# Performance work log

Measured on AMD Instinct MI355X. Metric: run time of the kernel, lower is better.

## Reference

```python
import jax, jax.numpy as jnp
import numpy as np

B, S, H = 8, 2048, 1024

def setup_inputs() -> dict:
    key = jax.random.key(0)
    k1, k2, k3, k4, k5, k6 = jax.random.split(key, 6)
    scale = 1.0 / np.sqrt(H)
    return {
        "hidden_states": jax.random.normal(k1, (B, S, H), dtype=jnp.float32),
        "key_padding_mask": jax.random.bernoulli(k2, 0.1, (B, S)),  # True = padded key
        "Wq_w": jax.random.normal(k3, (H, H), dtype=jnp.float32) * scale,
        "Wq_b": jax.random.normal(k4, (H,), dtype=jnp.float32) * 0.01,
        "Wk_w": jax.random.normal(k5, (H, H), dtype=jnp.float32) * scale,
        "Wk_b": jax.random.normal(k6, (H,), dtype=jnp.float32) * 0.01,
    }

def reference(hidden_states, key_padding_mask, Wq_w, Wq_b, Wk_w, Wk_b):
    # torch nn.Linear: y = x @ W.T + b
    q = jnp.einsum("bsh,oh->bso", hidden_states, Wq_w) + Wq_b
    k = jnp.einsum("bsh,oh->bso", hidden_states, Wk_w) + Wk_b
    d = q.shape[-1]
    scores = jnp.einsum("bqd,bkd->bqk", q, k) / jnp.sqrt(jnp.asarray(d, q.dtype))
    # scores[mask] -= inf  -> masked key columns become -inf
    scores = jnp.where(key_padding_mask[:, None, :], -jnp.inf, scores)
    attn = jax.nn.softmax(scores, axis=2)  # [B, S, S]
    out = jnp.einsum("bqk,bkd->bqd", attn, hidden_states)  # values = hidden_states (no proj)
    return out
```

## Files before the change

kernel.cpp:

```cpp
#include <hip/hip_runtime.h>
#include <hip/hip_bf16.h>

using bf16 = __hip_bfloat16;

using frag_ab = __attribute__((ext_vector_type(8))) short;
using frag_cd = __attribute__((ext_vector_type(4))) float;

#define TM 128
#define TN 128
#define TK 32

__device__ __forceinline__ unsigned short f2bu(float f) {
    bf16 h = __float2bfloat16(f);
    return *(unsigned short*)&h;
}

__device__ __forceinline__ void st_c(float* p, float v) { *p = v; }
__device__ __forceinline__ void st_c(bf16* p, float v)  { *p = __float2bfloat16(v); }

__device__ __forceinline__ void load16(const bf16* g, bf16* l) {
    __builtin_amdgcn_global_load_lds(
        (const __attribute__((address_space(1))) unsigned int*)g,
        (__attribute__((address_space(3))) unsigned int*)l,
        16, 0, 0);
}

template <typename TC, bool HAS_BIAS, bool MASK>
__global__ __launch_bounds__(256)
void mfma_gemm_nt(const bf16* __restrict__ A, const bf16* __restrict__ B,
                  const float* __restrict__ bias, const int* __restrict__ mask,
                  TC* __restrict__ C, int N, int K, int lda, int ldb, int ldc,
                  long sA, long sB, long sC, long sM, float scale)
{
    __shared__ bf16 As[2][TM][TK];
    __shared__ bf16 Bs[2][TN][TK];

    const int bz = blockIdx.z;
    const bf16* Ab = A + (long)bz * sA;
    const bf16* Bb = B + (long)bz * sB;
    TC* Cb = C + (long)bz * sC;
    const int* maskb = MASK ? (mask + (long)bz * sM) : nullptr;

    const int t  = threadIdx.x;
    const int m0 = blockIdx.x * TM;
    const int n0 = blockIdx.y * TN;

    const int srow  = t >> 2;
    const int skoff = (t & 3) << 3;
    const bf16* ga0 = Ab + (long)(m0 + srow) * lda + skoff;
    const bf16* ga1 = ga0 + (long)64 * lda;
    const bf16* gb0 = Bb + (long)(n0 + srow) * ldb + skoff;
    const bf16* gb1 = gb0 + (long)64 * ldb;

    const int wave = t >> 6;
    const int lane = t & 63;
    const int wm   = (wave & 1) * 64;
    const int wn   = (wave >> 1) * 64;
    const int lrow = lane & 15;
    const int quad = lane >> 4;

    frag_cd acc[4][4] = {};

#define STAGE(buf)                                         \
    do {                                                   \
        load16(ga0, &As[buf][srow][skoff]);                \
        load16(ga1, &As[buf][srow + 64][skoff]);           \
        load16(gb0, &Bs[buf][srow][skoff]);                \
        load16(gb1, &Bs[buf][srow + 64][skoff]);           \
        ga0 += TK; ga1 += TK; gb0 += TK; gb1 += TK;        \
    } while (0)

    STAGE(0);
    __syncthreads();

    int cur = 0;
    for (int k0 = 0; k0 < K; k0 += TK) {
        if (k0 + TK < K) STAGE(cur ^ 1);

        frag_ab af[4], bfv[4];
#pragma unroll
        for (int i = 0; i < 4; ++i)
            af[i] = *(const frag_ab*)&As[cur][wm + i * 16 + lrow][quad * 8];
#pragma unroll
        for (int j = 0; j < 4; ++j)
            bfv[j] = *(const frag_ab*)&Bs[cur][wn + j * 16 + lrow][quad * 8];
#pragma unroll
        for (int i = 0; i < 4; ++i)
#pragma unroll
            for (int j = 0; j < 4; ++j)
                acc[i][j] = __builtin_amdgcn_mfma_f32_16x16x32_bf16(
                    af[i], bfv[j], acc[i][j], 0, 0, 0);

        __syncthreads();
        cur ^= 1;
    }
#undef STAGE

#pragma unroll
    for (int j = 0; j < 4; ++j) {
        const int col = n0 + wn + j * 16 + lrow;
        const float bv = HAS_BIAS ? bias[col] : 0.0f;
        const bool msk = MASK ? (maskb[col] != 0) : false;
#pragma unroll
        for (int i = 0; i < 4; ++i) {
            const int rbase = m0 + wm + i * 16 + quad * 4;
#pragma unroll
            for (int r = 0; r < 4; ++r) {
                float v = acc[i][j][r] * scale + bv;
                if (MASK && msk) v = -INFINITY;
                st_c(&Cb[(long)(rbase + r) * ldc + col], v);
            }
        }
    }
}

__global__ __launch_bounds__(256)
void convert_transpose(const float* __restrict__ X, bf16* __restrict__ Xb,
                       bf16* __restrict__ XT, int S, int H)
{
    __shared__ unsigned short tile[64][72];
    const int b = blockIdx.z;
    const float* Xp = X + (long)b * S * H;
    bf16* Xbp = Xb + (long)b * S * H;
    bf16* XTp = XT + (long)b * H * S;
    const int h0 = blockIdx.x * 64, s0 = blockIdx.y * 64;
    const int t = threadIdx.x;
    const int r  = t >> 4;
    const int c4 = (t & 15) * 4;

#pragma unroll
    for (int p = 0; p < 4; ++p) {
        const int row = r + p * 16;
        const float4 v = *(const float4*)&Xp[(long)(s0 + row) * H + h0 + c4];
        ushort4 u;
        u.x = f2bu(v.x); u.y = f2bu(v.y); u.z = f2bu(v.z); u.w = f2bu(v.w);
        *(ushort4*)&tile[row][c4] = u;
        *(ushort4*)&Xbp[(long)(s0 + row) * H + h0 + c4] = u;
    }
    __syncthreads();
#pragma unroll
    for (int p = 0; p < 4; ++p) {
        const int hrow = r + p * 16;
        ushort4 u;
        u.x = tile[c4 + 0][hrow];
        u.y = tile[c4 + 1][hrow];
        u.z = tile[c4 + 2][hrow];
        u.w = tile[c4 + 3][hrow];
        *(ushort4*)&XTp[(long)(h0 + hrow) * S + s0 + c4] = u;
    }
}

__global__ __launch_bounds__(256)
void convert_bf16(const float* __restrict__ in, bf16* __restrict__ out, int n4)
{
    const int i = blockIdx.x * 256 + threadIdx.x;
    if (i < n4) {
        const float4 v = ((const float4*)in)[i];
        ushort4 u;
        u.x = f2bu(v.x); u.y = f2bu(v.y); u.z = f2bu(v.z); u.w = f2bu(v.w);
        ((ushort4*)out)[i] = u;
    }
}

__global__ __launch_bounds__(256)
void pack_bias(const float* __restrict__ qb, const float* __restrict__ kb,
               float* __restrict__ out, int H)
{
    const int i = blockIdx.x * 256 + threadIdx.x;
    out[i] = (i < H) ? qb[i] : kb[i - H];
}

__global__ __launch_bounds__(256)
void softmax_kernel(bf16* __restrict__ Smat, int Slen)
{
    const int row = blockIdx.x;
    bf16* srow = Smat + (long)row * Slen;

    const int t    = threadIdx.x;
    const int lane = t & 63;
    const int wid  = t >> 6;

    ushort4 u0 = ((const ushort4*)srow)[t * 2];
    ushort4 u1 = ((const ushort4*)srow)[t * 2 + 1];

    float vals[8];
    {
        const unsigned short us[8] = {u0.x, u0.y, u0.z, u0.w, u1.x, u1.y, u1.z, u1.w};
#pragma unroll
        for (int i = 0; i < 8; ++i) {
            unsigned int w = (unsigned int)us[i] << 16;
            vals[i] = *(float*)&w;
        }
    }

    float mx = vals[0];
#pragma unroll
    for (int i = 1; i < 8; ++i) mx = fmaxf(mx, vals[i]);

    __shared__ float red[4];
#pragma unroll
    for (int o = 32; o > 0; o >>= 1) mx = fmaxf(mx, __shfl_xor(mx, o, 64));
    if (lane == 0) red[wid] = mx;
    __syncthreads();
    mx = fmaxf(fmaxf(red[0], red[1]), fmaxf(red[2], red[3]));
    __syncthreads();

    float sum = 0.0f;
#pragma unroll
    for (int i = 0; i < 8; ++i) {
        const float e = __expf(vals[i] - mx);
        vals[i] = e;
        sum += e;
    }
#pragma unroll
    for (int o = 32; o > 0; o >>= 1) sum += __shfl_xor(sum, o, 64);
    if (lane == 0) red[wid] = sum;
    __syncthreads();
    sum = red[0] + red[1] + red[2] + red[3];

    const float inv = 1.0f / sum;
    ushort4 o0, o1;
    o0.x = f2bu(vals[0] * inv); o0.y = f2bu(vals[1] * inv);
    o0.z = f2bu(vals[2] * inv); o0.w = f2bu(vals[3] * inv);
    o1.x = f2bu(vals[4] * inv); o1.y = f2bu(vals[5] * inv);
    o1.z = f2bu(vals[6] * inv); o1.w = f2bu(vals[7] * inv);
    ((ushort4*)srow)[t * 2]     = o0;
    ((ushort4*)srow)[t * 2 + 1] = o1;
}

extern "C" void kernel_launch(void* const* d_in, const int* in_sizes, int n_in,
                              void* d_out, int out_size, void* d_ws, size_t ws_size,
                              hipStream_t stream)
{
    const float* hidden = (const float*)d_in[0];
    const int*   mask   = (const int*)d_in[1];
    const float* Wq_w   = (const float*)d_in[2];
    const float* Wq_b   = (const float*)d_in[3];
    const float* Wk_w   = (const float*)d_in[4];
    const float* Wk_b   = (const float*)d_in[5];
    float* out = (float*)d_out;

    const int B = 8, S = 2048, H = 1024;
    const int M = B * S;
    const long MH = (long)M * H;

    bf16* QK  = (bf16*)d_ws;
    bf16* XbT = QK + MH * 2;
    bf16* Sb  = XbT + MH;
    bf16* Xb  = Sb;
    bf16* Wb  = Xb + MH;
    float* biasP = (float*)(Wb + 2L * H * H);

    const dim3 blk(256);

    convert_transpose<<<dim3(H / 64, S / 64, B), blk, 0, stream>>>(hidden, Xb, XbT, S, H);
    convert_bf16<<<dim3(H * H / 1024), blk, 0, stream>>>(Wq_w, Wb, H * H / 4);
    convert_bf16<<<dim3(H * H / 1024), blk, 0, stream>>>(Wk_w, Wb + (long)H * H, H * H / 4);
    pack_bias<<<dim3(2 * H / 256), blk, 0, stream>>>(Wq_b, Wk_b, biasP, H);

    mfma_gemm_nt<bf16, true, false><<<dim3(M / TM, 2 * H / TN, 1), blk, 0, stream>>>(
        Xb, Wb, biasP, nullptr, QK, 2 * H, H, H, H, 2 * H, 0, 0, 0, 0, 1.0f);

    mfma_gemm_nt<bf16, false, true><<<dim3(S / TM, S / TN, B), blk, 0, stream>>>(
        QK, QK + H, nullptr, mask, Sb, S, H, 2 * H, 2 * H, S,
        (long)S * 2 * H, (long)S * 2 * H, (long)S * S, S, 1.0f / 32.0f);

    softmax_kernel<<<dim3(B * S), blk, 0, stream>>>(Sb, S);

    mfma_gemm_nt<float, false, false><<<dim3(S / TM, H / TN, B), blk, 0, stream>>>(
        Sb, XbT, nullptr, nullptr, out, H, S, S, S, H,
        (long)S * S, (long)H * S, (long)S * H, 0, 1.0f);
}
```

Baseline: 455.7 us.

## Swizzle GEMM shared-memory tiles, raise occupancy hint, merge weight conversions

Applies an XOR-like rotation to the 16-byte chunk index when staging A/B tiles into LDS via global_load_lds, and reads fragments with the matching rotated offset, to reduce LDS bank conflicts on the MFMA fragment loads. Adds a min-blocks-per-CU hint of 4 to the GEMM launch bounds, which may force register limits. Merges the two weight conversion kernels into one launch to save launch overhead. The swizzle must stay consistent between writer and reader or results break.

After: 415.9 us. -8.7%, faster.

```diff
diff --git a/kernel.cpp b/kernel.cpp
--- a/kernel.cpp
+++ b/kernel.cpp
@@ -26,7 +26,7 @@
 }
 
 template <typename TC, bool HAS_BIAS, bool MASK>
-__global__ __launch_bounds__(256)
+__global__ __launch_bounds__(256, 4)
 void mfma_gemm_nt(const bf16* __restrict__ A, const bf16* __restrict__ B,
                   const float* __restrict__ bias, const int* __restrict__ mask,
                   TC* __restrict__ C, int N, int K, int lda, int ldb, int ldc,
@@ -45,11 +45,13 @@
     const int m0 = blockIdx.x * TM;
     const int n0 = blockIdx.y * TN;
 
-    const int srow  = t >> 2;
-    const int skoff = (t & 3) << 3;
-    const bf16* ga0 = Ab + (long)(m0 + srow) * lda + skoff;
+    const int srow = t >> 2;
+    const int c    = t & 3;
+    const int gco  = (((c - (srow >> 1)) & 3) << 3);
+    const int lco  = c << 3;
+    const bf16* ga0 = Ab + (long)(m0 + srow) * lda + gco;
     const bf16* ga1 = ga0 + (long)64 * lda;
-    const bf16* gb0 = Bb + (long)(n0 + srow) * ldb + skoff;
+    const bf16* gb0 = Bb + (long)(n0 + srow) * ldb + gco;
     const bf16* gb1 = gb0 + (long)64 * ldb;
 
     const int wave = t >> 6;
@@ -58,15 +60,16 @@
     const int wn   = (wave >> 1) * 64;
     const int lrow = lane & 15;
     const int quad = lane >> 4;
+    const int rco  = (((quad + (lrow >> 1)) & 3) << 3);
 
     frag_cd acc[4][4] = {};
 
 #define STAGE(buf)                                         \
     do {                                                   \
-        load16(ga0, &As[buf][srow][skoff]);                \
-        load16(ga1, &As[buf][srow + 64][skoff]);           \
-        load16(gb0, &Bs[buf][srow][skoff]);                \
-        load16(gb1, &Bs[buf][srow + 64][skoff]);           \
+        load16(ga0, &As[buf][srow][lco]);                  \
+        load16(ga1, &As[buf][srow + 64][lco]);             \
+        load16(gb0, &Bs[buf][srow][lco]);                  \
+        load16(gb1, &Bs[buf][srow + 64][lco]);             \
         ga0 += TK; ga1 += TK; gb0 += TK; gb1 += TK;        \
     } while (0)
 
@@ -80,10 +83,10 @@
         frag_ab af[4], bfv[4];
 #pragma unroll
         for (int i = 0; i < 4; ++i)
-            af[i] = *(const frag_ab*)&As[cur][wm + i * 16 + lrow][quad * 8];
+            af[i] = *(const frag_ab*)&As[cur][wm + i * 16 + lrow][rco];
 #pragma unroll
         for (int j = 0; j < 4; ++j)
-            bfv[j] = *(const frag_ab*)&Bs[cur][wn + j * 16 + lrow][quad * 8];
+            bfv[j] = *(const frag_ab*)&Bs[cur][wn + j * 16 + lrow][rco];
 #pragma unroll
         for (int i = 0; i < 4; ++i)
 #pragma unroll
@@ -151,15 +154,17 @@
 }
 
 __global__ __launch_bounds__(256)
-void convert_bf16(const float* __restrict__ in, bf16* __restrict__ out, int n4)
+void convert_w2(const float* __restrict__ wa, const float* __restrict__ wb,
+                bf16* __restrict__ out, int n4each)
 {
     const int i = blockIdx.x * 256 + threadIdx.x;
-    if (i < n4) {
-        const float4 v = ((const float4*)in)[i];
-        ushort4 u;
-        u.x = f2bu(v.x); u.y = f2bu(v.y); u.z = f2bu(v.z); u.w = f2bu(v.w);
-        ((ushort4*)out)[i] = u;
-    }
+    const bool second = i >= n4each;
+    const float* src = second ? wb : wa;
+    const int j = second ? i - n4each : i;
+    const float4 v = ((const float4*)src)[j];
+    ushort4 u;
+    u.x = f2bu(v.x); u.y = f2bu(v.y); u.z = f2bu(v.z); u.w = f2bu(v.w);
+    ((ushort4*)out)[i] = u;
 }
 
 __global__ __launch_bounds__(256)
@@ -254,8 +259,7 @@
     const dim3 blk(256);
 
     convert_transpose<<<dim3(H / 64, S / 64, B), blk, 0, stream>>>(hidden, Xb, XbT, S, H);
-    convert_bf16<<<dim3(H * H / 1024), blk, 0, stream>>>(Wq_w, Wb, H * H / 4);
-    convert_bf16<<<dim3(H * H / 1024), blk, 0, stream>>>(Wk_w, Wb + (long)H * H, H * H / 4);
+    convert_w2<<<dim3(2 * H * H / 1024), blk, 0, stream>>>(Wq_w, Wk_w, Wb, H * H / 4);
     pack_bias<<<dim3(2 * H / 256), blk, 0, stream>>>(Wq_b, Wk_b, biasP, H);
 
     mfma_gemm_nt<bf16, true, false><<<dim3(M / TM, 2 * H / TN, 1), blk, 0, stream>>>(
```
